# Kernel optimization log

Hardware: AMD Instinct MI355X
Metric: run time of the kernel (lower is better)

The kernel has to match this reference:

```python
import jax, jax.numpy as jnp
import numpy as np

N_VER = 163842
IN_FEATS = 64
OUT_FEATS = 64


def setup_inputs() -> dict:
    key = jax.random.key(0)
    k1, k2, k3, k4 = jax.random.split(key, 4)
    x = jax.random.normal(k1, (N_VER, IN_FEATS), dtype=jnp.float32)
    hex_in = jax.random.randint(k2, (N_VER * 7,), 0, N_VER, dtype=jnp.int64)
    # Linear(7*in_feats, out_feats): weight stored as [7*in_feats, out_feats]
    W = jax.random.normal(k3, (7 * IN_FEATS, OUT_FEATS), dtype=jnp.float32) * (1.0 / np.sqrt(7 * IN_FEATS))
    b = jax.random.normal(k4, (OUT_FEATS,), dtype=jnp.float32) * 0.01
    return {"x": x, "hex_in": hex_in, "W": W, "b": b}


def reference(x, hex_in, W, b):
    n_ver = x.shape[0]
    # Gather 7-ring neighbor features: [7*n_ver, in_feats] -> [n_ver, 7*in_feats]
    x_new = x[hex_in].reshape(n_ver, 7 * x.shape[1])
    # Dense linear layer
    return x_new @ W + b
```

## Files before the change

kernel.cpp:

```cpp
#include <hip/hip_runtime.h>

#define N_VERT 163842
#define N8_X   1310736
#define RPB    256
#define GRID_MAIN ((N_VERT + RPB - 1) / RPB)

typedef float  f32x4  __attribute__((ext_vector_type(4)));
typedef short  s16x8  __attribute__((ext_vector_type(8)));

__device__ __forceinline__ unsigned short f2bf(float f) {
  union { float f; unsigned int u; } c; c.f = f;
  unsigned int u = c.u;
  u += 0x7FFFu + ((u >> 16) & 1u);
  return (unsigned short)(u >> 16);
}

__device__ __forceinline__ s16x8 cvt8(const f32x4 a, const f32x4 b) {
  s16x8 h;
  h[0] = (short)f2bf(a[0]); h[1] = (short)f2bf(a[1]);
  h[2] = (short)f2bf(a[2]); h[3] = (short)f2bf(a[3]);
  h[4] = (short)f2bf(b[0]); h[5] = (short)f2bf(b[1]);
  h[6] = (short)f2bf(b[2]); h[7] = (short)f2bf(b[3]);
  return h;
}

__global__ void detect64(const unsigned int* __restrict__ hexw, int* __restrict__ flag) {
  __shared__ int any;
  if (threadIdx.x == 0) any = 0;
  __syncthreads();
  if (hexw[2 * threadIdx.x + 1] != 0u) any = 1;
  __syncthreads();
  if (threadIdx.x == 0) *flag = (any == 0) ? 1 : 0;
}

__global__ __launch_bounds__(256) void prep(
    const float* __restrict__ x, const unsigned int* __restrict__ hexw,
    const float* __restrict__ W,
    unsigned short* __restrict__ Wf, unsigned short* __restrict__ xbf,
    int* __restrict__ flag)
{
  const int b = blockIdx.x, tid = threadIdx.x;

  if (b == 0) {
    __shared__ int any;
    if (tid == 0) any = 0;
    __syncthreads();
    if (hexw[2 * tid + 1] != 0u) any = 1;
    __syncthreads();
    if (tid == 0) *flag = (any == 0) ? 1 : 0;
  }
  if (b >= 1 && b <= 112) {
    const int t   = (b - 1) * 256 + tid;
    const int e   = t & 7;
    const int col = (t >> 3) & 63;
    const int hi  = (t >> 9) & 3;
    const int ks  = t >> 11;
    Wf[t] = f2bf(W[(ks * 32 + hi * 8 + e) * 64 + col]);
  }
  const int stride = gridDim.x * 256;
  for (int i = b * 256 + tid; i < N8_X; i += stride) {
    const f32x4* s = (const f32x4*)(x + (size_t)i * 8);
    *(s16x8*)(xbf + (size_t)i * 8) = cvt8(s[0], s[1]);
  }
}

template <int BF>
__global__ __launch_bounds__(512, 4) void hexconv3(
    const void* __restrict__ xsrc,
    const unsigned int* __restrict__ hexw,
    const void* __restrict__ wsrc,
    const float* __restrict__ bias,
    float* __restrict__ out,
    const int* __restrict__ flag)
{
  __shared__ unsigned short Wl[28672];
  __shared__ unsigned int   offb[RPB * 7];

  const int tid = threadIdx.x;
  const int wv  = tid >> 6;
  const int ln  = tid & 63;
  const int lo  = ln & 15;
  const int hi  = ln >> 4;
  const int vbase = blockIdx.x * RPB;
  const int is64  = flag ? *flag : 1;

  if (BF) {
    const s16x8* wsv = (const s16x8*)wsrc;
#pragma unroll
    for (int it = 0; it < 7; ++it)
      ((s16x8*)Wl)[it * 512 + tid] = wsv[it * 512 + tid];
  } else {
    const float* W = (const float*)wsrc;
    for (int it = 0; it < 56; ++it) {
      const int t   = it * 512 + tid;
      const int e   = t & 7;
      const int col = (t >> 3) & 63;
      const int hif = (t >> 9) & 3;
      const int ks  = t >> 11;
      Wl[t] = f2bf(W[(ks * 32 + hif * 8 + e) * 64 + col]);
    }
  }

#pragma unroll
  for (int it = 0; it < 4; ++it) {
    const int g = it * 512 + tid;
    if (g < RPB * 7) {
      unsigned int ib = 0;
      const int v = g / 7;
      if (vbase + v < N_VERT) {
        const unsigned int r = (unsigned int)vbase * 7 + g;
        ib = hexw[r << is64] << (BF ? 7 : 8);
      }
      offb[g] = ib;
    }
  }
  __syncthreads();

  const int r0 = wv * 32 + lo, r1 = r0 + 16;
  unsigned int off0[7], off1[7];
#pragma unroll
  for (int j = 0; j < 7; ++j) { off0[j] = offb[r0 * 7 + j]; off1[j] = offb[r1 * 7 + j]; }

  const char* xbase = (const char*)xsrc;
  const char* Wb    = (const char*)Wl + (hi * 64 + lo) * 16;

  f32x4 acc0[4], acc1[4];
#pragma unroll
  for (int nt = 0; nt < 4; ++nt) { acc0[nt] = (f32x4){0,0,0,0}; acc1[nt] = (f32x4){0,0,0,0}; }

  s16x8 a[2][2][2];
#define LOAD_A(par, jj)                                                        \
  do {                                                                         \
    const char* p0 = xbase + off0[jj];                                         \
    const char* p1 = xbase + off1[jj];                                         \
    if (BF) {                                                                  \
      a[par][0][0] = *(const s16x8*)(p0 + hi * 16);                            \
      a[par][1][0] = *(const s16x8*)(p0 + 64 + hi * 16);                       \
      a[par][0][1] = *(const s16x8*)(p1 + hi * 16);                            \
      a[par][1][1] = *(const s16x8*)(p1 + 64 + hi * 16);                       \
    } else {                                                                   \
      const f32x4* q0 = (const f32x4*)(p0 + hi * 32);                          \
      const f32x4* q1 = (const f32x4*)(p1 + hi * 32);                          \
      a[par][0][0] = cvt8(q0[0], q0[1]);                                       \
      a[par][1][0] = cvt8(*(const f32x4*)(p0 + 128 + hi * 32),                 \
                          *(const f32x4*)(p0 + 144 + hi * 32));                \
      a[par][0][1] = cvt8(q1[0], q1[1]);                                       \
      a[par][1][1] = cvt8(*(const f32x4*)(p1 + 128 + hi * 32),                 \
                          *(const f32x4*)(p1 + 144 + hi * 32));                \
    }                                                                          \
  } while (0)

  LOAD_A(0, 0);

#pragma unroll
  for (int j = 0; j < 7; ++j) {
    const int cur = j & 1, nxt = cur ^ 1;
    if (j < 6) LOAD_A(nxt, j + 1);
#pragma unroll
    for (int kss = 0; kss < 2; ++kss) {
#pragma unroll
      for (int nt = 0; nt < 4; ++nt) {
        const s16x8 bf = *(const s16x8*)(Wb + (2 * j + kss) * 4096 + nt * 256);
        acc0[nt] = __builtin_amdgcn_mfma_f32_16x16x32_bf16(a[cur][kss][0], bf, acc0[nt], 0, 0, 0);
        acc1[nt] = __builtin_amdgcn_mfma_f32_16x16x32_bf16(a[cur][kss][1], bf, acc1[nt], 0, 0, 0);
      }
    }
  }
#undef LOAD_A

  float bval[4];
#pragma unroll
  for (int nt = 0; nt < 4; ++nt) bval[nt] = bias[nt * 16 + lo];

  const int rbase = vbase + wv * 32;
#pragma unroll
  for (int i = 0; i < 4; ++i) {
    const int row0 = rbase + hi * 4 + i;
    if (row0 < N_VERT) {
      float* orow = out + (size_t)row0 * 64;
#pragma unroll
      for (int nt = 0; nt < 4; ++nt) orow[nt * 16 + lo] = acc0[nt][i] + bval[nt];
    }
    const int row1 = rbase + 16 + hi * 4 + i;
    if (row1 < N_VERT) {
      float* orow = out + (size_t)row1 * 64;
#pragma unroll
      for (int nt = 0; nt < 4; ++nt) orow[nt * 16 + lo] = acc1[nt][i] + bval[nt];
    }
  }
}

extern "C" void kernel_launch(void* const* d_in, const int* in_sizes, int n_in,
                              void* d_out, int out_size, void* d_ws, size_t ws_size,
                              hipStream_t stream) {
  const float*        x    = (const float*)d_in[0];
  const unsigned int* hexw = (const unsigned int*)d_in[1];
  const float*        W    = (const float*)d_in[2];
  const float*        b    = (const float*)d_in[3];
  float*              out  = (float*)d_out;

  const size_t WS_NEED = 65536 + (size_t)N_VERT * 64 * 2;

  if (ws_size >= WS_NEED) {
    int*            flag = (int*)d_ws;
    unsigned short* Wf   = (unsigned short*)((char*)d_ws + 4096);
    unsigned short* xbf  = (unsigned short*)((char*)d_ws + 65536);
    prep<<<2048, 256, 0, stream>>>(x, hexw, W, Wf, xbf, flag);
    hexconv3<1><<<GRID_MAIN, 512, 0, stream>>>(xbf, hexw, Wf, b, out, flag);
  } else {
    int* flag = (ws_size >= 4) ? (int*)d_ws : nullptr;
    if (flag) detect64<<<1, 256, 0, stream>>>(hexw, flag);
    hexconv3<0><<<GRID_MAIN, 512, 0, stream>>>(x, hexw, W, b, out, flag);
  }
}
```

Baseline: 45.58 us.

## Make gather-GEMM kernel persistent with cross-chunk software pipelining of neighbor loads

The main kernel becomes persistent: 512 blocks of 8 waves, each wave looping over 16-row chunks with a stride of 4096 chunks. Weights are staged into LDS once per block rather than once per 256 rows. The shared-memory offset staging is removed; each wave reads its own hex indices straight from global memory and prefetches the next chunk's indices and first gathered rows so loads overlap the MFMAs. Each wave now handles 16 rows per iteration instead of 32, so fewer independent MFMA chains hide latency, and the loop adds per-iteration control overhead.

Result: slower. 150.7 us (+230.7%).

```diff
diff --git a/kernel.cpp b/kernel.cpp
--- a/kernel.cpp
+++ b/kernel.cpp
@@ -2,8 +2,10 @@
 
 #define N_VERT 163842
 #define N8_X   1310736
-#define RPB    256
-#define GRID_MAIN ((N_VERT + RPB - 1) / RPB)
+#define CH     16
+#define NCH    10241
+#define NBLK   512
+#define NWAVE  4096
 
 typedef float  f32x4  __attribute__((ext_vector_type(4)));
 typedef short  s16x8  __attribute__((ext_vector_type(8)));
@@ -65,7 +67,7 @@
 }
 
 template <int BF>
-__global__ __launch_bounds__(512, 4) void hexconv3(
+__global__ __launch_bounds__(512, 4) void hexconv4(
     const void* __restrict__ xsrc,
     const unsigned int* __restrict__ hexw,
     const void* __restrict__ wsrc,
@@ -74,15 +76,13 @@
     const int* __restrict__ flag)
 {
   __shared__ unsigned short Wl[28672];
-  __shared__ unsigned int   offb[RPB * 7];
 
   const int tid = threadIdx.x;
   const int wv  = tid >> 6;
   const int ln  = tid & 63;
   const int lo  = ln & 15;
   const int hi  = ln >> 4;
-  const int vbase = blockIdx.x * RPB;
-  const int is64  = flag ? *flag : 1;
+  const int is64 = flag ? *flag : 1;
 
   if (BF) {
     const s16x8* wsv = (const s16x8*)wsrc;
@@ -100,94 +100,103 @@
       Wl[t] = f2bf(W[(ks * 32 + hif * 8 + e) * 64 + col]);
     }
   }
-
-#pragma unroll
-  for (int it = 0; it < 4; ++it) {
-    const int g = it * 512 + tid;
-    if (g < RPB * 7) {
-      unsigned int ib = 0;
-      const int v = g / 7;
-      if (vbase + v < N_VERT) {
-        const unsigned int r = (unsigned int)vbase * 7 + g;
-        ib = hexw[r << is64] << (BF ? 7 : 8);
-      }
-      offb[g] = ib;
-    }
-  }
   __syncthreads();
-
-  const int r0 = wv * 32 + lo, r1 = r0 + 16;
-  unsigned int off0[7], off1[7];
-#pragma unroll
-  for (int j = 0; j < 7; ++j) { off0[j] = offb[r0 * 7 + j]; off1[j] = offb[r1 * 7 + j]; }
 
   const char* xbase = (const char*)xsrc;
   const char* Wb    = (const char*)Wl + (hi * 64 + lo) * 16;
 
-  f32x4 acc0[4], acc1[4];
-#pragma unroll
-  for (int nt = 0; nt < 4; ++nt) { acc0[nt] = (f32x4){0,0,0,0}; acc1[nt] = (f32x4){0,0,0,0}; }
-
-  s16x8 a[2][2][2];
-#define LOAD_A(par, jj)                                                        \
+  float bval[4];
+#pragma unroll
+  for (int nt = 0; nt < 4; ++nt) bval[nt] = bias[nt * 16 + lo];
+
+  const unsigned int istep = 4u << is64;
+
+#define LOAD_OFF(dst, cc)                                                      \
   do {                                                                         \
-    const char* p0 = xbase + off0[jj];                                         \
-    const char* p1 = xbase + off1[jj];                                         \
+    int rr = (cc) * CH + lo;                                                   \
+    rr = (rr < N_VERT) ? rr : (N_VERT - 1);                                    \
+    const char* ip = (const char*)hexw + (unsigned long long)((unsigned)rr * 7u) * istep; \
+    _Pragma("unroll")                                                          \
+    for (int j = 0; j < 7; ++j)                                                \
+      (dst)[j] = *(const unsigned int*)(ip + j * istep);                       \
+  } while (0)
+
+#define LOAD_A(s, offarr, j)                                                   \
+  do {                                                                         \
+    const char* p = xbase + ((unsigned long long)(offarr)[j] << (BF ? 7 : 8)); \
     if (BF) {                                                                  \
-      a[par][0][0] = *(const s16x8*)(p0 + hi * 16);                            \
-      a[par][1][0] = *(const s16x8*)(p0 + 64 + hi * 16);                       \
-      a[par][0][1] = *(const s16x8*)(p1 + hi * 16);                            \
-      a[par][1][1] = *(const s16x8*)(p1 + 64 + hi * 16);                       \
+      s##_0 = *(const s16x8*)(p + hi * 16);                                    \
+      s##_1 = *(const s16x8*)(p + 64 + hi * 16);                               \
     } else {                                                                   \
-      const f32x4* q0 = (const f32x4*)(p0 + hi * 32);                          \
-      const f32x4* q1 = (const f32x4*)(p1 + hi * 32);                          \
-      a[par][0][0] = cvt8(q0[0], q0[1]);                                       \
-      a[par][1][0] = cvt8(*(const f32x4*)(p0 + 128 + hi * 32),                 \
-                          *(const f32x4*)(p0 + 144 + hi * 32));                \
-      a[par][0][1] = cvt8(q1[0], q1[1]);                                       \
-      a[par][1][1] = cvt8(*(const f32x4*)(p1 + 128 + hi * 32),                 \
-                          *(const f32x4*)(p1 + 144 + hi * 32));                \
+      const f32x4* q0 = (const f32x4*)(p + hi * 32);                           \
+      s##_0 = cvt8(q0[0], q0[1]);                                              \
+      s##_1 = cvt8(*(const f32x4*)(p + 128 + hi * 32),                         \
+                   *(const f32x4*)(p + 144 + hi * 32));                        \
     }                                                                          \
   } while (0)
 
-  LOAD_A(0, 0);
-
-#pragma unroll
-  for (int j = 0; j < 7; ++j) {
-    const int cur = j & 1, nxt = cur ^ 1;
-    if (j < 6) LOAD_A(nxt, j + 1);
-#pragma unroll
-    for (int kss = 0; kss < 2; ++kss) {
-#pragma unroll
-      for (int nt = 0; nt < 4; ++nt) {
-        const s16x8 bf = *(const s16x8*)(Wb + (2 * j + kss) * 4096 + nt * 256);
-        acc0[nt] = __builtin_amdgcn_mfma_f32_16x16x32_bf16(a[cur][kss][0], bf, acc0[nt], 0, 0, 0);
-        acc1[nt] = __builtin_amdgcn_mfma_f32_16x16x32_bf16(a[cur][kss][1], bf, acc1[nt], 0, 0, 0);
+#define MFMA_J(jj, s)                                                          \
+  do {                                                                         \
+    _Pragma("unroll")                                                          \
+    for (int nt = 0; nt < 4; ++nt) {                                           \
+      const s16x8 bf0 = *(const s16x8*)(Wb + (2 * (jj)) * 4096 + nt * 256);    \
+      acc[nt] = __builtin_amdgcn_mfma_f32_16x16x32_bf16(s##_0, bf0, acc[nt], 0, 0, 0); \
+    }                                                                          \
+    _Pragma("unroll")                                                          \
+    for (int nt = 0; nt < 4; ++nt) {                                           \
+      const s16x8 bf1 = *(const s16x8*)(Wb + (2 * (jj) + 1) * 4096 + nt * 256);\
+      acc[nt] = __builtin_amdgcn_mfma_f32_16x16x32_bf16(s##_1, bf1, acc[nt], 0, 0, 0); \
+    }                                                                          \
+  } while (0)
+
+  unsigned int offc[7], offn[7];
+  s16x8 a0_0, a0_1, a1_0, a1_1, a2_0, a2_1;
+
+  int c  = blockIdx.x * 8 + wv;
+  int cn = c + NWAVE;
+  LOAD_OFF(offc, c);
+  { const int cc = (cn < NCH) ? cn : (NCH - 1); LOAD_OFF(offn, cc); }
+  LOAD_A(a0, offc, 0);
+  LOAD_A(a1, offc, 1);
+
+  while (true) {
+    f32x4 acc[4];
+#pragma unroll
+    for (int nt = 0; nt < 4; ++nt) acc[nt] = (f32x4){0.f, 0.f, 0.f, 0.f};
+
+    LOAD_A(a2, offc, 2);  MFMA_J(0, a0);
+    LOAD_A(a0, offc, 3);  MFMA_J(1, a1);
+    LOAD_A(a1, offc, 4);  MFMA_J(2, a2);
+    LOAD_A(a2, offc, 5);  MFMA_J(3, a0);
+    LOAD_A(a0, offc, 6);  MFMA_J(4, a1);
+    LOAD_A(a1, offn, 0);  MFMA_J(5, a2);
+    LOAD_A(a2, offn, 1);  MFMA_J(6, a0);
+
+    const int vb = c * CH;
+#pragma unroll
+    for (int i = 0; i < 4; ++i) {
+      const int row = vb + hi * 4 + i;
+      if (row < N_VERT) {
+        float* orow = out + (size_t)row * 64;
+#pragma unroll
+        for (int nt = 0; nt < 4; ++nt) orow[nt * 16 + lo] = acc[nt][i] + bval[nt];
       }
     }
-  }
+
+    c = cn;
+    if (c >= NCH) break;
+    cn = c + NWAVE;
+
+    a0_0 = a1_0; a0_1 = a1_1;
+    a1_0 = a2_0; a1_1 = a2_1;
+#pragma unroll
+    for (int j = 0; j < 7; ++j) offc[j] = offn[j];
+    const int cc = (cn < NCH) ? cn : (NCH - 1);
+    LOAD_OFF(offn, cc);
+  }
+#undef LOAD_OFF
 #undef LOAD_A
-
-  float bval[4];
-#pragma unroll
-  for (int nt = 0; nt < 4; ++nt) bval[nt] = bias[nt * 16 + lo];
-
-  const int rbase = vbase + wv * 32;
-#pragma unroll
-  for (int i = 0; i < 4; ++i) {
-    const int row0 = rbase + hi * 4 + i;
-    if (row0 < N_VERT) {
-      float* orow = out + (size_t)row0 * 64;
-#pragma unroll
-      for (int nt = 0; nt < 4; ++nt) orow[nt * 16 + lo] = acc0[nt][i] + bval[nt];
-    }
-    const int row1 = rbase + 16 + hi * 4 + i;
-    if (row1 < N_VERT) {
-      float* orow = out + (size_t)row1 * 64;
-#pragma unroll
-      for (int nt = 0; nt < 4; ++nt) orow[nt * 16 + lo] = acc1[nt][i] + bval[nt];
-    }
-  }
+#undef MFMA_J
 }
 
 extern "C" void kernel_launch(void* const* d_in, const int* in_sizes, int n_in,
@@ -206,10 +215,10 @@
     unsigned short* Wf   = (unsigned short*)((char*)d_ws + 4096);
     unsigned short* xbf  = (unsigned short*)((char*)d_ws + 65536);
     prep<<<2048, 256, 0, stream>>>(x, hexw, W, Wf, xbf, flag);
-    hexconv3<1><<<GRID_MAIN, 512, 0, stream>>>(xbf, hexw, Wf, b, out, flag);
+    hexconv4<1><<<NBLK, 512, 0, stream>>>(xbf, hexw, Wf, b, out, flag);
   } else {
     int* flag = (ws_size >= 4) ? (int*)d_ws : nullptr;
     if (flag) detect64<<<1, 256, 0, stream>>>(hexw, flag);
-    hexconv3<0><<<GRID_MAIN, 512, 0, stream>>>(x, hexw, W, b, out, flag);
-  }
-}
+    hexconv4<0><<<NBLK, 512, 0, stream>>>(x, hexw, W, b, out, flag);
+  }
+}
```
